# Kernel tuning notes

Measured on AMD Instinct MI355X. Metric: run time of the kernel, lower is better.

The kernel has to match this reference:

```python
import jax, jax.numpy as jnp
import numpy as np

N = 50000   # nodes
E = 600000  # edges (both relations mixed)
D = 128     # in_features == out_features


def _gcn(x, W, b, row, col, w, n):
    """PyG GCNConv: add self-loops (weight 1), symmetric normalization, linear, aggregate, bias.
    Edges with w==0 contribute nothing to degree or messages (== masked subgraph)."""
    idx = jnp.arange(n)
    srow = jnp.concatenate([row, idx])
    scol = jnp.concatenate([col, idx])
    sw = jnp.concatenate([w, jnp.ones((n,), x.dtype)])
    deg = jax.ops.segment_sum(sw, scol, num_segments=n)                 # [n]
    dinv = jnp.where(deg > 0, jax.lax.rsqrt(jnp.maximum(deg, 1e-12)), 0.0)
    norm = dinv[srow] * sw * dinv[scol]                                 # [E+n]
    h = x @ W                                                           # [n, D]
    out = jax.ops.segment_sum(h[srow] * norm[:, None], scol, num_segments=n)
    return out + b


def setup_inputs() -> dict:
    key = jax.random.key(0)
    ks = jax.random.split(key, 12)
    s_in = 1.0 / np.sqrt(D)
    s_g = 1.0 / np.sqrt(3 * D)
    return {
        "x": jax.random.normal(ks[0], (N, D), dtype=jnp.float32),
        "edge_index": jax.random.randint(ks[1], (2, E), 0, N, dtype=jnp.int64),
        "edge_type": jax.random.randint(ks[2], (E,), 0, 2, dtype=jnp.int64),
        "W_sl": jax.random.normal(ks[3], (D, D), dtype=jnp.float32) * s_in,
        "b_sl": jnp.zeros((D,), jnp.float32),
        "W0": jax.random.normal(ks[4], (D, D), dtype=jnp.float32) * s_in,
        "b0": jnp.zeros((D,), jnp.float32),
        "W1": jax.random.normal(ks[5], (D, D), dtype=jnp.float32) * s_in,
        "b1": jnp.zeros((D,), jnp.float32),
        "W_g": jax.random.normal(ks[6], (3 * D, D), dtype=jnp.float32) * s_g,
        "b_g": jnp.zeros((D,), jnp.float32),
    }


def reference(x, edge_index, edge_type, W_sl, b_sl, W0, b0, W1, b1, W_g, b_g):
    n = x.shape[0]
    row, col = edge_index[0], edge_index[1]
    x_x = x @ W_sl + b_sl                                   # self-loop linear
    w0 = (edge_type == 0).astype(x.dtype)
    w1 = (edge_type == 1).astype(x.dtype)
    x_n = _gcn(x, W0, b0, row, col, w0, n)                  # relation 0 GCN
    x_d = _gcn(x, W1, b1, row, col, w1, n)                  # relation 1 GCN
    gat_raw = jax.nn.softmax(jnp.concatenate([x_x, x_n, x_d], axis=1) @ W_g + b_g, axis=-1)
    gat = jnp.cumsum(gat_raw, axis=-1)                      # ordered-neuron gate
    return x_d[:, ::-1] * gat + x_x + x_n
```

## Files before the change

### kernel.cpp

```cpp
#include <hip/hip_runtime.h>
#include <hip/hip_bf16.h>
#include <hip/hip_fp16.h>
#include <math.h>


typedef __attribute__((ext_vector_type(8))) short bf16x8;
typedef __attribute__((ext_vector_type(4))) float f32x4;
typedef __attribute__((ext_vector_type(8))) unsigned short ushort8;

__device__ inline float b2f(unsigned short u) {
  return __uint_as_float(((unsigned)u) << 16);
}
__device__ inline unsigned short f2bf(float f) {
  __hip_bfloat16 b = __float2bfloat16(f);
  return *reinterpret_cast<unsigned short*>(&b);
}

__global__ __launch_bounds__(256) void pack_count(const float* __restrict__ Wsl,
                                                  const float* __restrict__ W0,
                                                  const float* __restrict__ W1,
                                                  const float* __restrict__ Wg,
                                                  unsigned short* __restrict__ Wp3,
                                                  unsigned short* __restrict__ Wgp,
                                                  const int* __restrict__ col,
                                                  const int* __restrict__ etype,
                                                  int* __restrict__ deg,
                                                  int* __restrict__ erank, int E, int n) {
  if (blockIdx.x < 48) {
    int tid = blockIdx.x * 256 + threadIdx.x;
    if (tid < 6144) {
      int z = tid / 2048, r = tid % 2048;
      int lane = r & 63, idx = r >> 6;
      int kf = idx & 3, ct = idx >> 2;
      const float* W = (z == 0) ? Wsl : (z == 1) ? W0 : W1;
      unsigned short* dst = Wp3 + (size_t)z * 16384 + (size_t)r * 8;
      int krow = kf * 32 + (lane >> 4) * 8;
      int ccol = ct * 16 + (lane & 15);
#pragma unroll
      for (int j = 0; j < 8; ++j) dst[j] = f2bf(W[(size_t)(krow + j) * 128 + ccol]);
    } else {
      int r = tid - 6144;
      int lane = r & 63, idx = r >> 6;
      int kf = idx % 12, ct = idx / 12;
      unsigned short* dst = Wgp + (size_t)r * 8;
      int krow = kf * 32 + (lane >> 4) * 8;
      int ccol = ct * 16 + (lane & 15);
#pragma unroll
      for (int j = 0; j < 8; ++j) dst[j] = f2bf(Wg[(size_t)(krow + j) * 128 + ccol]);
    }
  } else {
    int e = (blockIdx.x - 48) * 256 + threadIdx.x;
    if (e >= E) return;
    int rk = atomicAdd(&deg[(size_t)etype[e] * n + col[e]], 1);
    erank[e] = rk;
  }
}

__global__ __launch_bounds__(256) void dinv_scan1(const int* __restrict__ deg,
                                                  float* __restrict__ dinv,
                                                  int* __restrict__ partials,
                                                  int n2, int nb) {
  int tid = threadIdx.x;
  if ((int)blockIdx.x < nb) {
    int base = blockIdx.x * 2048 + tid * 8;
    int s = 0;
#pragma unroll
    for (int k = 0; k < 8; ++k) {
      int i = base + k;
      if (i < n2) s += deg[i];
    }
    __shared__ int sb[256];
    sb[tid] = s;
    __syncthreads();
    for (int o = 128; o; o >>= 1) {
      if (tid < o) sb[tid] += sb[tid + o];
      __syncthreads();
    }
    if (tid == 0) partials[blockIdx.x] = sb[0];
  } else {
    int i = (blockIdx.x - nb) * 256 + tid;
    if (i < n2) dinv[i] = rsqrtf((float)deg[i] + 1.0f);
  }
}

__global__ __launch_bounds__(256) void scan3b(const int* __restrict__ partials,
                                              const int* __restrict__ deg,
                                              int* __restrict__ row_start, int n2, int nb) {
  __shared__ int sb[256];
  __shared__ int ex[256];
  int tid = threadIdx.x;
  int pv = (tid < nb) ? partials[tid] : 0;
  sb[tid] = pv;
  __syncthreads();
  for (int o = 1; o < 256; o <<= 1) {
    int t = (tid >= o) ? sb[tid - o] : 0;
    __syncthreads();
    sb[tid] += t;
    __syncthreads();
  }
  ex[tid] = sb[tid] - pv;
  __syncthreads();
  int base = ex[blockIdx.x];
  __syncthreads();

  int bstart = blockIdx.x * 2048 + tid * 8;
  int v[8];
  int s = 0;
#pragma unroll
  for (int k = 0; k < 8; ++k) {
    int i = bstart + k;
    v[k] = (i < n2) ? deg[i] : 0;
    s += v[k];
  }
  sb[tid] = s;
  __syncthreads();
  for (int o = 1; o < 256; o <<= 1) {
    int t = (tid >= o) ? sb[tid - o] : 0;
    __syncthreads();
    sb[tid] += t;
    __syncthreads();
  }
  int run = base + (sb[tid] - s);
#pragma unroll
  for (int k = 0; k < 8; ++k) {
    int i = bstart + k;
    if (i < n2) {
      row_start[i] = run;
      run += v[k];
    }
  }
}

__global__ __launch_bounds__(256) void gemm3_fill(
    const float* __restrict__ x, const unsigned short* __restrict__ Wp3,
    const float* __restrict__ bsl, unsigned short* __restrict__ hx,
    unsigned short* __restrict__ h0, unsigned short* __restrict__ h1,
    const int* __restrict__ row, const int* __restrict__ col,
    const int* __restrict__ etype, const int* __restrict__ erank,
    const int* __restrict__ row_start, const float* __restrict__ dinv,
    unsigned int* __restrict__ ebuf, int n, int E, int gb) {
  __shared__ unsigned short xs[64 * 136];
  int tid = threadIdx.x;
  if ((int)blockIdx.x >= gb) {
    int e = (blockIdx.x - gb) * 256 + tid;
    if (e >= E) return;
    int r = row[e], c = col[e], t = etype[e];
    int b = t * n + c;
    float nrm = dinv[t * n + r] * dinv[b];
    int pos = row_start[b] + erank[e];
    unsigned int rec = (unsigned int)(r & 0xFFFF) |
                       ((unsigned int)__half_as_ushort(__float2half_rn(nrm)) << 16);
    ebuf[pos] = rec;
    return;
  }
  int row0 = blockIdx.x * 64;
  {
    const float4* xg = (const float4*)(x + (size_t)row0 * 128);
    int maxv = (n - row0) * 32;
#pragma unroll
    for (int i = 0; i < 8; ++i) {
      int idx = tid + i * 256;
      float4 v = {0.f, 0.f, 0.f, 0.f};
      if (idx < maxv) v = xg[idx];
      int rr = idx >> 5, c4 = idx & 31;
      ushort4 u;
      u.x = f2bf(v.x);
      u.y = f2bf(v.y);
      u.z = f2bf(v.z);
      u.w = f2bf(v.w);
      *(ushort4*)&xs[rr * 136 + c4 * 4] = u;
    }
  }
  __syncthreads();
  int w = tid >> 6;
  int l = tid & 63;
  int q = l >> 4;
  int c = l & 15;
  bf16x8 af[4];
#pragma unroll
  for (int kf = 0; kf < 4; ++kf)
    af[kf] = *(const bf16x8*)&xs[(w * 16 + c) * 136 + kf * 32 + q * 8];
  __syncthreads();

#pragma unroll
  for (int z = 0; z < 3; ++z) {
    const bf16x8* Bp = (const bf16x8*)(Wp3 + (size_t)z * 16384);
    unsigned short* h = (z == 0) ? hx : (z == 1) ? h0 : h1;
#pragma unroll
    for (int ct = 0; ct < 8; ++ct) {
      f32x4 acc = {0.f, 0.f, 0.f, 0.f};
#pragma unroll
      for (int kf = 0; kf < 4; ++kf)
        acc = __builtin_amdgcn_mfma_f32_16x16x32_bf16(af[kf], Bp[(ct * 4 + kf) * 64 + l], acc, 0, 0, 0);
      int fc = ct * 16 + c;
      float bias = (z == 0) ? bsl[fc] : 0.f;
#pragma unroll
      for (int i = 0; i < 4; ++i)
        xs[(w * 16 + q * 4 + i) * 136 + fc] = f2bf(acc[i] + bias);
    }
    __syncthreads();
#pragma unroll
    for (int i = 0; i < 4; ++i) {
      int idx = tid + i * 256;
      int rr = idx >> 4, c8 = idx & 15;
      int gr = row0 + rr;
      if (gr < n)
        *(ushort8*)(h + (size_t)gr * 128 + c8 * 8) = *(const ushort8*)&xs[rr * 136 + c8 * 8];
    }
    __syncthreads();
  }
}

__global__ __launch_bounds__(256) void gather2(const unsigned short* __restrict__ h0,
                                               const unsigned short* __restrict__ h1,
                                               const unsigned int* __restrict__ ebuf,
                                               const int* __restrict__ row_start,
                                               const int* __restrict__ deg,
                                               const float* __restrict__ dinv,
                                               const float* __restrict__ b0,
                                               const float* __restrict__ b1,
                                               unsigned short* __restrict__ xn,
                                               unsigned short* __restrict__ xd, int n) {
  int t = blockIdx.y;
  long long gid = (long long)blockIdx.x * 256 + threadIdx.x;
  int node = (int)(gid >> 3);
  if (node >= n) return;
  int sub = (int)(gid & 7);
  const ushort8* hp8 = (const ushort8*)(t ? h1 : h0);
  const float* bias = t ? b1 : b0;
  unsigned short* out = t ? xd : xn;
  const int* rs = row_start + (size_t)t * n;
  const int* dg = deg + (size_t)t * n;
  float di = dinv[(size_t)t * n + node];

  float accA[8], accB[8];
  float acc2A[8] = {0, 0, 0, 0, 0, 0, 0, 0}, acc2B[8] = {0, 0, 0, 0, 0, 0, 0, 0};
  {
    ushort8 sa = hp8[(size_t)node * 16 + sub * 2];
    ushort8 sbv = hp8[(size_t)node * 16 + sub * 2 + 1];
    float sl = di * di;
#pragma unroll
    for (int k = 0; k < 8; ++k) {
      accA[k] = fmaf(b2f(sa[k]), sl, bias[sub * 16 + k]);
      accB[k] = fmaf(b2f(sbv[k]), sl, bias[sub * 16 + 8 + k]);
    }
  }
  int s = rs[node];
  int e = s + dg[node];
  int j = s;
  for (; j + 1 < e; j += 2) {
    unsigned int r0 = ebuf[j], r1 = ebuf[j + 1];
    int i0 = (int)(r0 & 0xFFFFu), i1 = (int)(r1 & 0xFFFFu);
    float n0 = __half2float(__ushort_as_half((unsigned short)(r0 >> 16)));
    float n1 = __half2float(__ushort_as_half((unsigned short)(r1 >> 16)));
    ushort8 v0a = hp8[(size_t)i0 * 16 + sub * 2];
    ushort8 v0b = hp8[(size_t)i0 * 16 + sub * 2 + 1];
    ushort8 v1a = hp8[(size_t)i1 * 16 + sub * 2];
    ushort8 v1b = hp8[(size_t)i1 * 16 + sub * 2 + 1];
#pragma unroll
    for (int k = 0; k < 8; ++k) {
      accA[k] = fmaf(b2f(v0a[k]), n0, accA[k]);
      accB[k] = fmaf(b2f(v0b[k]), n0, accB[k]);
      acc2A[k] = fmaf(b2f(v1a[k]), n1, acc2A[k]);
      acc2B[k] = fmaf(b2f(v1b[k]), n1, acc2B[k]);
    }
  }
  if (j < e) {
    unsigned int r0 = ebuf[j];
    int i0 = (int)(r0 & 0xFFFFu);
    float n0 = __half2float(__ushort_as_half((unsigned short)(r0 >> 16)));
    ushort8 v0a = hp8[(size_t)i0 * 16 + sub * 2];
    ushort8 v0b = hp8[(size_t)i0 * 16 + sub * 2 + 1];
#pragma unroll
    for (int k = 0; k < 8; ++k) {
      accA[k] = fmaf(b2f(v0a[k]), n0, accA[k]);
      accB[k] = fmaf(b2f(v0b[k]), n0, accB[k]);
    }
  }
  ushort8 ua, ub;
#pragma unroll
  for (int k = 0; k < 8; ++k) {
    ua[k] = f2bf(accA[k] + acc2A[k]);
    ub[k] = f2bf(accB[k] + acc2B[k]);
  }
  ((ushort8*)out)[(size_t)node * 16 + sub * 2] = ua;
  ((ushort8*)out)[(size_t)node * 16 + sub * 2 + 1] = ub;
}

__global__ __launch_bounds__(256) void gate_combine(
    const unsigned short* __restrict__ hx, const unsigned short* __restrict__ xn,
    const unsigned short* __restrict__ xd, const unsigned short* __restrict__ Wgp,
    const float* __restrict__ bg, float* __restrict__ out, int n) {
  __shared__ __align__(16) unsigned short Bs[2][8 * 64 * 8];
  int tid = threadIdx.x;
  int wv = tid >> 6;
  int l = tid & 63;
  int q = l >> 4;
  int c = l & 15;
  int row0 = blockIdx.x * 64 + wv * 16;
  int ar = row0 + c;
  if (ar > n - 1) ar = n - 1;
  bf16x8 af[12];
  {
    const unsigned short* p0 = hx + (size_t)ar * 128 + q * 8;
    const unsigned short* p1 = xn + (size_t)ar * 128 + q * 8;
    const unsigned short* p2 = xd + (size_t)ar * 128 + q * 8;
#pragma unroll
    for (int k = 0; k < 4; ++k) {
      af[k] = *(const bf16x8*)(p0 + k * 32);
      af[4 + k] = *(const bf16x8*)(p1 + k * 32);
      af[8 + k] = *(const bf16x8*)(p2 + k * 32);
    }
  }
  {
    int u = tid;
#pragma unroll
    for (int r = 0; r < 2; ++r, u += 256) {
      int ct = u >> 6, ll = u & 63;
      *(ushort8*)&Bs[0][u * 8] = *(const ushort8*)(Wgp + ((size_t)(ct * 12) * 64 + ll) * 8);
    }
  }
  __syncthreads();
  f32x4 acc[8];
#pragma unroll
  for (int ct = 0; ct < 8; ++ct) acc[ct] = (f32x4){0.f, 0.f, 0.f, 0.f};
#pragma unroll
  for (int kf = 0; kf < 12; ++kf) {
    int cur = kf & 1;
    if (kf < 11) {
      int u = tid;
#pragma unroll
      for (int r = 0; r < 2; ++r, u += 256) {
        int ct = u >> 6, ll = u & 63;
        *(ushort8*)&Bs[cur ^ 1][u * 8] =
            *(const ushort8*)(Wgp + ((size_t)(ct * 12 + kf + 1) * 64 + ll) * 8);
      }
    }
    bf16x8 a = af[kf];
#pragma unroll
    for (int ct = 0; ct < 8; ++ct)
      acc[ct] = __builtin_amdgcn_mfma_f32_16x16x32_bf16(
          a, *(const bf16x8*)&Bs[cur][(ct * 64 + l) * 8], acc[ct], 0, 0, 0);
    if (kf < 11) __syncthreads();
  }
#pragma unroll
  for (int ct = 0; ct < 8; ++ct) {
    float bgv = bg[ct * 16 + c];
#pragma unroll
    for (int i = 0; i < 4; ++i) acc[ct][i] += bgv;
  }
#pragma unroll
  for (int i = 0; i < 4; ++i) {
    float m = acc[0][i];
#pragma unroll
    for (int ct = 1; ct < 8; ++ct) m = fmaxf(m, acc[ct][i]);
#pragma unroll
    for (int o = 1; o < 16; o <<= 1) m = fmaxf(m, __shfl_xor(m, o));
    float e[8];
    float s = 0.f;
#pragma unroll
    for (int ct = 0; ct < 8; ++ct) {
      e[ct] = __expf(acc[ct][i] - m);
      s += e[ct];
    }
#pragma unroll
    for (int o = 1; o < 16; o <<= 1) s += __shfl_xor(s, o);
    float inv = 1.0f / s;
    int gr = row0 + q * 4 + i;
    float run = 0.f;
#pragma unroll
    for (int ct = 0; ct < 8; ++ct) {
      float p = e[ct];
#pragma unroll
      for (int o = 1; o < 16; o <<= 1) {
        float t = __shfl_up(p, o);
        if (c >= o) p += t;
      }
      float T = __shfl(p, q * 16 + 15);
      float gat = (run + p) * inv;
      run += T;
      int f = ct * 16 + c;
      if (gr < n) {
        size_t gb = (size_t)gr * 128;
        float xxv = b2f(hx[gb + f]);
        float xnv = b2f(xn[gb + f]);
        float xdv = b2f(xd[gb + 127 - f]);
        out[gb + f] = fmaf(xdv, gat, xxv + xnv);
      }
    }
  }
}

extern "C" void kernel_launch(void* const* d_in, const int* in_sizes, int n_in,
                              void* d_out, int out_size, void* d_ws, size_t ws_size,
                              hipStream_t stream) {
  const float* x = (const float*)d_in[0];
  const int* eidx = (const int*)d_in[1];
  const int* etype = (const int*)d_in[2];
  const float* Wsl = (const float*)d_in[3];
  const float* bsl = (const float*)d_in[4];
  const float* W0 = (const float*)d_in[5];
  const float* b0 = (const float*)d_in[6];
  const float* W1 = (const float*)d_in[7];
  const float* b1 = (const float*)d_in[8];
  const float* Wg = (const float*)d_in[9];
  const float* bg = (const float*)d_in[10];
  int n = in_sizes[0] / 128;
  int E = in_sizes[2];
  const int* row = eidx;
  const int* col = eidx + E;
  int n2 = 2 * n;

  char* w = (char*)d_ws;
  int* deg = (int*)w;             w += (size_t)n2 * 4;
  float* dinv = (float*)w;        w += (size_t)n2 * 4;
  int* row_start = (int*)w;       w += (size_t)n2 * 4;
  int* partials = (int*)w;        w += 1024;
  unsigned int* ebuf = (unsigned int*)w;  w += (size_t)E * 4;
  int* erank = (int*)w;           w += (size_t)E * 4;
  unsigned short* Wp3 = (unsigned short*)w;  w += 3 * 128 * 128 * 2;
  unsigned short* Wgp = (unsigned short*)w;  w += 384 * 128 * 2;
  unsigned short* hx = (unsigned short*)w;   w += (size_t)n * 128 * 2;
  unsigned short* h0 = (unsigned short*)w;   w += (size_t)n * 128 * 2;
  unsigned short* h1 = (unsigned short*)w;   w += (size_t)n * 128 * 2;
  unsigned short* xn = (unsigned short*)w;   w += (size_t)n * 128 * 2;
  unsigned short* xd = (unsigned short*)w;
  float* out = (float*)d_out;

  hipMemsetAsync(deg, 0, (size_t)n2 * 4, stream);

  int cd_blocks = (E + 255) / 256;
  pack_count<<<48 + cd_blocks, 256, 0, stream>>>(Wsl, W0, W1, Wg, Wp3, Wgp,
                                                 col, etype, deg, erank, E, n);
  int nb = (n2 + 2047) / 2048;
  dinv_scan1<<<nb + (n2 + 255) / 256, 256, 0, stream>>>(deg, dinv, partials, n2, nb);
  scan3b<<<nb, 256, 0, stream>>>(partials, deg, row_start, n2, nb);

  int gemm_blocks = (n + 63) / 64;
  gemm3_fill<<<gemm_blocks + cd_blocks, 256, 0, stream>>>(
      x, Wp3, bsl, hx, h0, h1, row, col, etype, erank, row_start, dinv, ebuf,
      n, E, gemm_blocks);

  int ga_blocks = (int)(((long long)n * 8 + 255) / 256);
  gather2<<<dim3(ga_blocks, 2), 256, 0, stream>>>(h0, h1, ebuf, row_start, deg, dinv,
                                                  b0, b1, xn, xd, n);
  gate_combine<<<(n + 63) / 64, 256, 0, stream>>>(hx, xn, xd, Wgp, bg, out, n);
}
```

Before: 146.3 us.

## Stage packed weight fragments through double-buffered LDS in gemm3_fill

The fused three-way GEMM previously had each wave read its B fragments for the packed weights straight from global memory. It now loads each k-slice of the packed weights cooperatively into a double-buffered shared-memory tile, prefetching the next slice while the MFMAs on the current one run. Each of the four waves no longer issues its own redundant global loads for the same weights. The cost is an extra 16 KB of LDS per block, which can lower occupancy, and a __syncthreads on every k-step.

```diff
diff --git a/kernel.cpp b/kernel.cpp
--- a/kernel.cpp
+++ b/kernel.cpp
@@ -140,6 +140,7 @@
     const int* __restrict__ row_start, const float* __restrict__ dinv,
     unsigned int* __restrict__ ebuf, int n, int E, int gb) {
   __shared__ unsigned short xs[64 * 136];
+  __shared__ __align__(16) unsigned short Bs[2][4096];
   int tid = threadIdx.x;
   if ((int)blockIdx.x >= gb) {
     int e = (blockIdx.x - gb) * 256 + tid;
@@ -170,6 +171,12 @@
       u.w = f2bf(v.w);
       *(ushort4*)&xs[rr * 136 + c4 * 4] = u;
     }
+    int u = tid;
+#pragma unroll
+    for (int r = 0; r < 2; ++r, u += 256) {
+      int ct = u >> 6, ll = u & 63;
+      *(ushort8*)&Bs[0][u * 8] = *(const ushort8*)(Wp3 + ((size_t)(ct * 4) * 64 + ll) * 8);
+    }
   }
   __syncthreads();
   int w = tid >> 6;
@@ -182,32 +189,52 @@
     af[kf] = *(const bf16x8*)&xs[(w * 16 + c) * 136 + kf * 32 + q * 8];
   __syncthreads();
 
-#pragma unroll
-  for (int z = 0; z < 3; ++z) {
-    const bf16x8* Bp = (const bf16x8*)(Wp3 + (size_t)z * 16384);
-    unsigned short* h = (z == 0) ? hx : (z == 1) ? h0 : h1;
-#pragma unroll
-    for (int ct = 0; ct < 8; ++ct) {
-      f32x4 acc = {0.f, 0.f, 0.f, 0.f};
-#pragma unroll
-      for (int kf = 0; kf < 4; ++kf)
-        acc = __builtin_amdgcn_mfma_f32_16x16x32_bf16(af[kf], Bp[(ct * 4 + kf) * 64 + l], acc, 0, 0, 0);
-      int fc = ct * 16 + c;
-      float bias = (z == 0) ? bsl[fc] : 0.f;
-#pragma unroll
-      for (int i = 0; i < 4; ++i)
-        xs[(w * 16 + q * 4 + i) * 136 + fc] = f2bf(acc[i] + bias);
-    }
-    __syncthreads();
-#pragma unroll
-    for (int i = 0; i < 4; ++i) {
-      int idx = tid + i * 256;
-      int rr = idx >> 4, c8 = idx & 15;
-      int gr = row0 + rr;
-      if (gr < n)
-        *(ushort8*)(h + (size_t)gr * 128 + c8 * 8) = *(const ushort8*)&xs[rr * 136 + c8 * 8];
-    }
-    __syncthreads();
+  f32x4 acc[8];
+#pragma unroll
+  for (int ct = 0; ct < 8; ++ct) acc[ct] = (f32x4){0.f, 0.f, 0.f, 0.f};
+#pragma unroll
+  for (int g = 0; g < 12; ++g) {
+    int z = g >> 2, kf = g & 3;
+    int cur = g & 1;
+    if (g < 11) {
+      int zn = (g + 1) >> 2, kfn = (g + 1) & 3;
+      int u = tid;
+#pragma unroll
+      for (int r = 0; r < 2; ++r, u += 256) {
+        int ct = u >> 6, ll = u & 63;
+        *(ushort8*)&Bs[cur ^ 1][u * 8] = *(const ushort8*)(
+            Wp3 + (size_t)zn * 16384 + ((size_t)(ct * 4 + kfn) * 64 + ll) * 8);
+      }
+    }
+    bf16x8 a = af[kf];
+#pragma unroll
+    for (int ct = 0; ct < 8; ++ct)
+      acc[ct] = __builtin_amdgcn_mfma_f32_16x16x32_bf16(
+          a, *(const bf16x8*)&Bs[cur][(ct * 64 + l) * 8], acc[ct], 0, 0, 0);
+    if (kf == 3) {
+      unsigned short* h = (z == 0) ? hx : (z == 1) ? h0 : h1;
+#pragma unroll
+      for (int ct = 0; ct < 8; ++ct) {
+        int fc = ct * 16 + c;
+        float bias = (z == 0) ? bsl[fc] : 0.f;
+#pragma unroll
+        for (int i = 0; i < 4; ++i)
+          xs[(w * 16 + q * 4 + i) * 136 + fc] = f2bf(acc[ct][i] + bias);
+        acc[ct] = (f32x4){0.f, 0.f, 0.f, 0.f};
+      }
+      __syncthreads();
+#pragma unroll
+      for (int i = 0; i < 4; ++i) {
+        int idx = tid + i * 256;
+        int rr = idx >> 4, c8 = idx & 15;
+        int gr = row0 + rr;
+        if (gr < n)
+          *(ushort8*)(h + (size_t)gr * 128 + c8 * 8) = *(const ushort8*)&xs[rr * 136 + c8 * 8];
+      }
+      __syncthreads();
+    } else {
+      __syncthreads();
+    }
   }
 }
 
@@ -291,7 +318,7 @@
     const unsigned short* __restrict__ hx, const unsigned short* __restrict__ xn,
     const unsigned short* __restrict__ xd, const unsigned short* __restrict__ Wgp,
     const float* __restrict__ bg, float* __restrict__ out, int n) {
-  __shared__ __align__(16) unsigned short Bs[2][8 * 64 * 8];
+  __shared__ __align__(16) unsigned short Bs[2][4096];
   int tid = threadIdx.x;
   int wv = tid >> 6;
   int l = tid & 63;
```

Result: faster. 127.9 us (-12.6%).
